# Kernel tuning notes

Measured on AMD Instinct MI355X. Metric: run time of the kernel, lower is better.

Reference implementation:

```python
import jax, jax.numpy as jnp
import numpy as np

B, C, H, W = 8, 64, 64, 64
CQ = C // 2

def setup_inputs() -> dict:
    key = jax.random.key(0)
    ks = jax.random.split(key, 10)
    s = 0.05
    return {
        "x": jax.random.normal(ks[0], (B, C, H, W), jnp.float32),
        "wq": jax.random.normal(ks[1], (CQ, C), jnp.float32) * s,
        "bq": jax.random.normal(ks[2], (CQ,), jnp.float32) * s,
        "wk": jax.random.normal(ks[3], (CQ, C), jnp.float32) * s,
        "bk": jax.random.normal(ks[4], (CQ,), jnp.float32) * s,
        "wv": jax.random.normal(ks[5], (C, C), jnp.float32) * s,
        "bv": jax.random.normal(ks[6], (C,), jnp.float32) * s,
        "wf": jax.random.normal(ks[7], (C, C), jnp.float32) * s,
        "bf": jax.random.normal(ks[8], (C,), jnp.float32) * s,
        "gamma": jnp.ones((1,), jnp.float32),
    }

def _conv1x1(w, b, x):
    # 1x1 conv == channel matmul: [O,C] x [B,C,H,W] -> [B,O,H,W]
    return jnp.einsum('oc,bchw->bohw', w, x) + b[None, :, None, None]

def reference(x, wq, bq, wk, bk, wv, bv, wf, bf, gamma):
    b, c, h, w = x.shape
    n = h * w
    q = _conv1x1(wq, bq, x).reshape(b, -1, n)   # [B, C/2, N]
    k = _conv1x1(wk, bk, x).reshape(b, -1, n)   # [B, C/2, N]
    v = _conv1x1(wv, bv, x).reshape(b, c, n)    # [B, C,   N]
    scale = 1.0 / jnp.sqrt(jnp.float32(n))
    energy = jnp.einsum('bcn,bcm->bnm', q, k) * scale  # [B, N, N]
    attn = jax.nn.softmax(energy, axis=-1)
    out = jnp.einsum('bcm,bnm->bcn', v, attn)          # V @ attn^T
    out = out.reshape(b, c, h, w)
    out = _conv1x1(wf, bf, out)
    return gamma[0] * out + x
```

## Files before the change

### kernel.cpp

```cpp
#include <hip/hip_runtime.h>

typedef unsigned short u16;
typedef unsigned int   u32;
typedef __bf16  bf16x8 __attribute__((ext_vector_type(8)));
typedef float   f32x16 __attribute__((ext_vector_type(16)));
typedef u32     u32x4  __attribute__((ext_vector_type(4)));

#define NN  4096
#define CCH 64
#define CQ  32
#define K1S 0.0225421092623961f

__device__ __forceinline__ u16 bfc(float a) { return __builtin_bit_cast(u16, (__bf16)a); }

__device__ __forceinline__ u32 e2pk_s(float a, float b, float& ps) {
  float ea, eb; u32 r;
  asm("v_exp_f32 %0, %1" : "=v"(ea) : "v"(a));
  asm("v_exp_f32 %0, %1" : "=v"(eb) : "v"(b));
  ps += ea + eb;
  asm("v_cvt_pk_bf16_f32 %0, %1, %2" : "=v"(r) : "v"(ea), "v"(eb));
  return r;
}

__device__ __forceinline__ void gload16(const void* g, void* l) {
  __builtin_amdgcn_global_load_lds((const __attribute__((address_space(1))) void*)g,
                                   (__attribute__((address_space(3))) void*)l, 16, 0, 0);
}


__global__ __launch_bounds__(512) void qkv_kernel(
    const float* __restrict__ x,
    const float* __restrict__ wq, const float* __restrict__ bq,
    const float* __restrict__ wk, const float* __restrict__ bk,
    const float* __restrict__ wv, const float* __restrict__ bv,
    u16* __restrict__ qT, char* __restrict__ kws, char* __restrict__ vws)
{
  __shared__ float xs[64][64];
  __shared__ u16 qls[64][34];
  __shared__ u16 kls[64][34];
  __shared__ u16 vls[64][66];
  const int bid = blockIdx.x;
  const int b = bid >> 6;
  const int chunk = bid & 63;
  const int nbase = chunk * 64;
  const int t = threadIdx.x, lane = t & 63, wid = t >> 6;

  {
    const float* xb = x + (size_t)b * CCH * NN + nbase;
    const int row = t >> 3, colq = (t & 7) * 2;
    float4 v0 = *(const float4*)(xb + (size_t)row * NN + colq * 4);
    float4 v1 = *(const float4*)(xb + (size_t)row * NN + colq * 4 + 4);
    float4* dst = (float4*)&xs[0][0];
    dst[row * 16 + colq]     = v0;
    dst[row * 16 + colq + 1] = v1;
  }
  __syncthreads();

  float xcol[64];
  #pragma unroll
  for (int c = 0; c < 64; ++c) xcol[c] = xs[c][lane];

  const float* w; const float* bias; float sc = 1.0f;
  const int sub = (wid & 1) * 16;
  if (wid < 2)      { w = wq + sub * 64; bias = bq + sub; sc = K1S; }
  else if (wid < 4) { w = wk + sub * 64; bias = bk + sub; }
  else              { w = wv + (wid - 4) * 16 * 64; bias = bv + (wid - 4) * 16; }

  #pragma unroll 2
  for (int i = 0; i < 16; ++i) {
    float a = bias[i];
    #pragma unroll
    for (int c = 0; c < 64; ++c) a = fmaf(w[i * 64 + c], xcol[c], a);
    a *= sc;
    u16 hv = bfc(a);
    if (wid < 2)      qls[lane][sub + i] = hv;
    else if (wid < 4) kls[lane][sub + i] = hv;
    else              vls[(wid - 4) * 16 + i][lane] = hv;
  }
  __syncthreads();

  u32* qdst = (u32*)(qT + ((size_t)b * NN + nbase) * CQ);
  #pragma unroll
  for (int jj = 0; jj < 2; ++jj) {
    int i = t + 512 * jj;
    int n = i >> 4, cp = i & 15;
    qdst[i] = *(const u32*)&qls[n][cp * 2];
  }
  u32* kimg = (u32*)(kws + ((size_t)b * 64 + chunk) * 4096);
  #pragma unroll
  for (int jj = 0; jj < 2; ++jj) {
    int i = t + 512 * jj;
    int reg = i >> 8, l = (i >> 2) & 63, j2 = i & 3;
    int s = reg >> 1, ks = reg & 1;
    int key = s * 32 + (l & 31);
    int ck  = ks * 16 + (l >> 5) * 8 + j2 * 2;
    kimg[i] = *(const u32*)&kls[key][ck];
  }
  u32* vimg = (u32*)(vws + ((size_t)b * 64 + chunk) * 8192);
  #pragma unroll
  for (int jj = 0; jj < 4; ++jj) {
    int i = t + 512 * jj;
    int reg = i >> 8, l = (i >> 2) & 63, j2 = i & 3;
    int s = reg >> 2, kb = (reg >> 1) & 1, ct = reg & 1;
    int c   = ct * 32 + (l & 31);
    int key = s * 32 + kb * 16 + (l >> 5) * 4 + (j2 >> 1) * 8 + (j2 & 1) * 2;
    vimg[i] = *(const u32*)&vls[c][key];
  }
}

template<int NSPLIT>
__global__ __launch_bounds__(256, 3) void attn_kernel(
    const u16* __restrict__ qT, const char* __restrict__ kws, const char* __restrict__ vws,
    u32* __restrict__ opart, float* __restrict__ lpart)
{
  constexpr int CH = 64 / NSPLIT;
  constexpr int MH = CH / 2;
  __shared__ __align__(16) char kbuf[2][8192];
  __shared__ __align__(16) char vbuf[2][16384];
  const int bid = blockIdx.x;
  const int b = bid & 7, qt = (bid >> 3) & 15, split = bid >> 7;
  const int t = threadIdx.x, lane = t & 63, wid = t >> 6;
  const int h = lane >> 5, c31 = lane & 31;

  const u16* qpA = qT + ((size_t)b * NN + qt * 256 + wid * 64 + c31) * CQ + h * 8;
  const bf16x8 qfA0 = *(const bf16x8*)(qpA);
  const bf16x8 qfA1 = *(const bf16x8*)(qpA + 16);
  const bf16x8 qfB0 = *(const bf16x8*)(qpA + 32 * CQ);
  const bf16x8 qfB1 = *(const bf16x8*)(qpA + 32 * CQ + 16);

  const char* ksrc = kws + ((size_t)b * 64 + split * CH) * 4096 + t * 16;
  const char* vsrc = vws + ((size_t)b * 64 + split * CH) * 8192 + t * 16;

  auto stage = [&](int buf, int m) {
    const char* kc = ksrc + (size_t)m * 8192;
    const char* vc = vsrc + (size_t)m * 16384;
    gload16(kc,         &kbuf[buf][wid * 1024]);
    gload16(kc + 4096,  &kbuf[buf][4096 + wid * 1024]);
    gload16(vc,         &vbuf[buf][wid * 1024]);
    gload16(vc + 4096,  &vbuf[buf][4096 + wid * 1024]);
    gload16(vc + 8192,  &vbuf[buf][8192 + wid * 1024]);
    gload16(vc + 12288, &vbuf[buf][12288 + wid * 1024]);
  };

  f32x16 accA0 = {}, accA1 = {}, accB0 = {}, accB1 = {};
  float lsumA = 0.f, lsumB = 0.f;
  const int lofs = lane * 16;

  stage(0, 0);

  #pragma unroll
  for (int m = 0; m < MH; ++m) {
    asm volatile("s_waitcnt vmcnt(0)" ::: "memory");
    __builtin_amdgcn_s_barrier();
    __builtin_amdgcn_sched_barrier(0);
    if (m + 1 < MH) stage((m + 1) & 1, m + 1);
    const int cur = m & 1;

    #pragma unroll
    for (int sub = 0; sub < 2; ++sub) {
      const char* kb = &kbuf[cur][sub * 4096];
      const char* vb = &vbuf[cur][sub * 8192];

      const bf16x8 kf0 = *(const bf16x8*)&kb[lofs];
      const bf16x8 kf1 = *(const bf16x8*)&kb[1024 + lofs];
      const bf16x8 kf2 = *(const bf16x8*)&kb[2048 + lofs];
      const bf16x8 kf3 = *(const bf16x8*)&kb[3072 + lofs];

      {
        f32x16 sA0, sA1;
        __builtin_amdgcn_s_setprio(1);
        sA0 = __builtin_amdgcn_mfma_f32_32x32x16_bf16(kf0, qfA0, (f32x16){}, 0, 0, 0);
        sA0 = __builtin_amdgcn_mfma_f32_32x32x16_bf16(kf1, qfA1, sA0, 0, 0, 0);
        sA1 = __builtin_amdgcn_mfma_f32_32x32x16_bf16(kf2, qfA0, (f32x16){}, 0, 0, 0);
        sA1 = __builtin_amdgcn_mfma_f32_32x32x16_bf16(kf3, qfA1, sA1, 0, 0, 0);
        __builtin_amdgcn_s_setprio(0);
        u32 pw[16] __attribute__((aligned(16)));
        #pragma unroll
        for (int r = 0; r < 16; r += 2) {
          pw[r >> 1]       = e2pk_s(sA0[r], sA0[r + 1], lsumA);
          pw[8 + (r >> 1)] = e2pk_s(sA1[r], sA1[r + 1], lsumA);
        }
        __builtin_amdgcn_s_setprio(1);
        #pragma unroll
        for (int s = 0; s < 2; ++s) {
          #pragma unroll
          for (int kb2 = 0; kb2 < 2; ++kb2) {
            const bf16x8 pf = __builtin_bit_cast(bf16x8, *(const u32x4*)&pw[s * 8 + kb2 * 4]);
            const bf16x8 vf0 = *(const bf16x8*)&vb[(s * 4 + kb2 * 2) * 1024 + lofs];
            const bf16x8 vf1 = *(const bf16x8*)&vb[(s * 4 + kb2 * 2 + 1) * 1024 + lofs];
            accA0 = __builtin_amdgcn_mfma_f32_32x32x16_bf16(vf0, pf, accA0, 0, 0, 0);
            accA1 = __builtin_amdgcn_mfma_f32_32x32x16_bf16(vf1, pf, accA1, 0, 0, 0);
          }
        }
        __builtin_amdgcn_s_setprio(0);
      }
      {
        f32x16 sB0, sB1;
        __builtin_amdgcn_s_setprio(1);
        sB0 = __builtin_amdgcn_mfma_f32_32x32x16_bf16(kf0, qfB0, (f32x16){}, 0, 0, 0);
        sB0 = __builtin_amdgcn_mfma_f32_32x32x16_bf16(kf1, qfB1, sB0, 0, 0, 0);
        sB1 = __builtin_amdgcn_mfma_f32_32x32x16_bf16(kf2, qfB0, (f32x16){}, 0, 0, 0);
        sB1 = __builtin_amdgcn_mfma_f32_32x32x16_bf16(kf3, qfB1, sB1, 0, 0, 0);
        __builtin_amdgcn_s_setprio(0);
        u32 pw[16] __attribute__((aligned(16)));
        #pragma unroll
        for (int r = 0; r < 16; r += 2) {
          pw[r >> 1]       = e2pk_s(sB0[r], sB0[r + 1], lsumB);
          pw[8 + (r >> 1)] = e2pk_s(sB1[r], sB1[r + 1], lsumB);
        }
        __builtin_amdgcn_s_setprio(1);
        #pragma unroll
        for (int s = 0; s < 2; ++s) {
          #pragma unroll
          for (int kb2 = 0; kb2 < 2; ++kb2) {
            const bf16x8 pf = __builtin_bit_cast(bf16x8, *(const u32x4*)&pw[s * 8 + kb2 * 4]);
            const bf16x8 vf0 = *(const bf16x8*)&vb[(s * 4 + kb2 * 2) * 1024 + lofs];
            const bf16x8 vf1 = *(const bf16x8*)&vb[(s * 4 + kb2 * 2 + 1) * 1024 + lofs];
            accB0 = __builtin_amdgcn_mfma_f32_32x32x16_bf16(vf0, pf, accB0, 0, 0, 0);
            accB1 = __builtin_amdgcn_mfma_f32_32x32x16_bf16(vf1, pf, accB1, 0, 0, 0);
          }
        }
        __builtin_amdgcn_s_setprio(0);
      }
    }
  }

  lsumA += __shfl_xor(lsumA, 32, 64);
  lsumB += __shfl_xor(lsumB, 32, 64);

  const int qt128 = qt * 2 + (wid >> 1);
  const size_t obase = ((size_t)(b * 32 + qt128) * NSPLIT + split) * 4096;
  #pragma unroll
  for (int j = 0; j < 2; ++j) {
    const int col = (wid & 1) * 64 + j * 32 + c31;
    #pragma unroll
    for (int ct = 0; ct < 2; ++ct) {
      const f32x16& a = j ? (ct ? accB1 : accB0) : (ct ? accA1 : accA0);
      #pragma unroll
      for (int g2 = 0; g2 < 4; ++g2) {
        #pragma unroll
        for (int b2 = 0; b2 < 2; ++b2) {
          int cp = ct * 16 + g2 * 4 + h * 2 + b2;
          float lo = a[g2 * 4 + b2 * 2], hi = a[g2 * 4 + b2 * 2 + 1];
          u32 pr; asm("v_cvt_pk_bf16_f32 %0, %1, %2" : "=v"(pr) : "v"(lo), "v"(hi));
          opart[obase + cp * 128 + col] = pr;
        }
      }
    }
    if (h == 0)
      lpart[((size_t)(b * 32 + qt128) * NSPLIT + split) * 128 + col] = j ? lsumB : lsumA;
  }
}

template<int NSPLIT>
__global__ __launch_bounds__(512) void combine_kernel(
    const u32* __restrict__ opart, const float* __restrict__ lpart,
    const float* __restrict__ x, const float* __restrict__ wf, const float* __restrict__ bfb,
    const float* __restrict__ gamma, float* __restrict__ out)
{
  __shared__ float ols[64][65];
  __shared__ float linv[64];
  const int bid = blockIdx.x;
  const int b = bid & 7, qt64 = bid >> 3;
  const int qt128 = qt64 >> 1, qh = qt64 & 1;
  const int t = threadIdx.x, lane = t & 63, wid = t >> 6;

  const u32* ob = opart + (size_t)(b * 32 + qt128) * NSPLIT * 4096 + qh * 64;
  #pragma unroll
  for (int jj = 0; jj < 4; ++jj) {
    int i = t + 512 * jj;
    int cp = i >> 6, q = i & 63;
    float lo = 0.f, hi = 0.f;
    #pragma unroll
    for (int s = 0; s < NSPLIT; ++s) {
      u32 a = ob[s * 4096 + cp * 128 + q];
      lo += __builtin_bit_cast(float, (a << 16));
      hi += __builtin_bit_cast(float, (a & 0xffff0000u));
    }
    ols[cp * 2][q]     = lo;
    ols[cp * 2 + 1][q] = hi;
  }
  if (t < 64) {
    const float* lp = lpart + (size_t)(b * 32 + qt128) * NSPLIT * 128 + qh * 64;
    float l = 0.f;
    #pragma unroll
    for (int s = 0; s < NSPLIT; ++s) l += lp[s * 128 + t];
    linv[t] = 1.f / l;
  }
  __syncthreads();

  const float oinv = linv[lane];
  float oc[64];
  #pragma unroll
  for (int c = 0; c < 64; ++c) oc[c] = ols[c][lane] * oinv;
  const float gm = gamma[0];
  const size_t nidx = (size_t)qt64 * 64 + lane;
  #pragma unroll
  for (int i = 0; i < 8; ++i) {
    const int o = wid * 8 + i;
    float a = bfb[o];
    #pragma unroll
    for (int c = 0; c < 64; ++c) a = fmaf(wf[o * 64 + c], oc[c], a);
    const size_t idx = ((size_t)b * CCH + o) * NN + nidx;
    out[idx] = gm * a + x[idx];
  }
}

extern "C" void kernel_launch(void* const* d_in, const int* in_sizes, int n_in,
                              void* d_out, int out_size, void* d_ws, size_t ws_size,
                              hipStream_t stream) {
  const float* x     = (const float*)d_in[0];
  const float* wq    = (const float*)d_in[1];
  const float* bq    = (const float*)d_in[2];
  const float* wk    = (const float*)d_in[3];
  const float* bk    = (const float*)d_in[4];
  const float* wv    = (const float*)d_in[5];
  const float* bv    = (const float*)d_in[6];
  const float* wf    = (const float*)d_in[7];
  const float* bf_   = (const float*)d_in[8];
  const float* gamma = (const float*)d_in[9];
  float* out = (float*)d_out;

  u16* qT   = (u16*)d_ws;
  char* kws = (char*)(qT + (size_t)8 * NN * CQ);
  char* vws = kws + (size_t)8 * 64 * 4096;
  u32* opart = (u32*)(vws + (size_t)8 * 64 * 8192);
  const size_t base = 2097152ull + 2097152ull + 4194304ull;
  const size_t need8 = base + 8ull * (4194304ull + 131072ull);
  const size_t need4 = base + 4ull * (4194304ull + 131072ull);

  qkv_kernel<<<dim3(512), dim3(512), 0, stream>>>(x, wq, bq, wk, bk, wv, bv, qT, kws, vws);
  if (ws_size >= need8) {
    float* lpart = (float*)(opart + (size_t)8 * 32 * 8 * 4096);
    attn_kernel<8><<<dim3(1024), dim3(256), 0, stream>>>(qT, kws, vws, opart, lpart);
    combine_kernel<8><<<dim3(512), dim3(512), 0, stream>>>(opart, lpart, x, wf, bf_, gamma, out);
  } else if (ws_size >= need4) {
    float* lpart = (float*)(opart + (size_t)8 * 32 * 4 * 4096);
    attn_kernel<4><<<dim3(512), dim3(256), 0, stream>>>(qT, kws, vws, opart, lpart);
    combine_kernel<4><<<dim3(512), dim3(512), 0, stream>>>(opart, lpart, x, wf, bf_, gamma, out);
  } else {
    float* lpart = (float*)(opart + (size_t)8 * 32 * 2 * 4096);
    attn_kernel<2><<<dim3(256), dim3(256), 0, stream>>>(qT, kws, vws, opart, lpart);
    combine_kernel<2><<<dim3(512), dim3(512), 0, stream>>>(opart, lpart, x, wf, bf_, gamma, out);
  }
}
```

Baseline: 94.41 us.

## Load K/V fragments directly to registers with double-buffered prefetch, drop LDS staging

Result: slower. 218.0 us (+130.9%).

```diff
diff --git a/kernel.cpp b/kernel.cpp
--- a/kernel.cpp
+++ b/kernel.cpp
@@ -20,11 +20,6 @@
   ps += ea + eb;
   asm("v_cvt_pk_bf16_f32 %0, %1, %2" : "=v"(r) : "v"(ea), "v"(eb));
   return r;
-}
-
-__device__ __forceinline__ void gload16(const void* g, void* l) {
-  __builtin_amdgcn_global_load_lds((const __attribute__((address_space(1))) void*)g,
-                                   (__attribute__((address_space(3))) void*)l, 16, 0, 0);
 }
 
 
@@ -109,14 +104,11 @@
 }
 
 template<int NSPLIT>
-__global__ __launch_bounds__(256, 3) void attn_kernel(
+__global__ __launch_bounds__(256, 2) void attn_kernel(
     const u16* __restrict__ qT, const char* __restrict__ kws, const char* __restrict__ vws,
     u32* __restrict__ opart, float* __restrict__ lpart)
 {
   constexpr int CH = 64 / NSPLIT;
-  constexpr int MH = CH / 2;
-  __shared__ __align__(16) char kbuf[2][8192];
-  __shared__ __align__(16) char vbuf[2][16384];
   const int bid = blockIdx.x;
   const int b = bid & 7, qt = (bid >> 3) & 15, split = bid >> 7;
   const int t = threadIdx.x, lane = t & 63, wid = t >> 6;
@@ -128,101 +120,88 @@
   const bf16x8 qfB0 = *(const bf16x8*)(qpA + 32 * CQ);
   const bf16x8 qfB1 = *(const bf16x8*)(qpA + 32 * CQ + 16);
 
-  const char* ksrc = kws + ((size_t)b * 64 + split * CH) * 4096 + t * 16;
-  const char* vsrc = vws + ((size_t)b * 64 + split * CH) * 8192 + t * 16;
-
-  auto stage = [&](int buf, int m) {
-    const char* kc = ksrc + (size_t)m * 8192;
-    const char* vc = vsrc + (size_t)m * 16384;
-    gload16(kc,         &kbuf[buf][wid * 1024]);
-    gload16(kc + 4096,  &kbuf[buf][4096 + wid * 1024]);
-    gload16(vc,         &vbuf[buf][wid * 1024]);
-    gload16(vc + 4096,  &vbuf[buf][4096 + wid * 1024]);
-    gload16(vc + 8192,  &vbuf[buf][8192 + wid * 1024]);
-    gload16(vc + 12288, &vbuf[buf][12288 + wid * 1024]);
-  };
+  const char* kcb = kws + ((size_t)b * 64 + split * CH) * 4096 + lane * 16;
+  const char* vcb = vws + ((size_t)b * 64 + split * CH) * 8192 + lane * 16;
 
   f32x16 accA0 = {}, accA1 = {}, accB0 = {}, accB1 = {};
   float lsumA = 0.f, lsumB = 0.f;
-  const int lofs = lane * 16;
-
-  stage(0, 0);
-
-  #pragma unroll
-  for (int m = 0; m < MH; ++m) {
-    asm volatile("s_waitcnt vmcnt(0)" ::: "memory");
-    __builtin_amdgcn_s_barrier();
-    __builtin_amdgcn_sched_barrier(0);
-    if (m + 1 < MH) stage((m + 1) & 1, m + 1);
-    const int cur = m & 1;
-
-    #pragma unroll
-    for (int sub = 0; sub < 2; ++sub) {
-      const char* kb = &kbuf[cur][sub * 4096];
-      const char* vb = &vbuf[cur][sub * 8192];
-
-      const bf16x8 kf0 = *(const bf16x8*)&kb[lofs];
-      const bf16x8 kf1 = *(const bf16x8*)&kb[1024 + lofs];
-      const bf16x8 kf2 = *(const bf16x8*)&kb[2048 + lofs];
-      const bf16x8 kf3 = *(const bf16x8*)&kb[3072 + lofs];
-
-      {
-        f32x16 sA0, sA1;
-        __builtin_amdgcn_s_setprio(1);
-        sA0 = __builtin_amdgcn_mfma_f32_32x32x16_bf16(kf0, qfA0, (f32x16){}, 0, 0, 0);
-        sA0 = __builtin_amdgcn_mfma_f32_32x32x16_bf16(kf1, qfA1, sA0, 0, 0, 0);
-        sA1 = __builtin_amdgcn_mfma_f32_32x32x16_bf16(kf2, qfA0, (f32x16){}, 0, 0, 0);
-        sA1 = __builtin_amdgcn_mfma_f32_32x32x16_bf16(kf3, qfA1, sA1, 0, 0, 0);
-        __builtin_amdgcn_s_setprio(0);
-        u32 pw[16] __attribute__((aligned(16)));
+
+  bf16x8 Ka[4], Va[8], Kb[4], Vb[8];
+
+  auto ldK = [&](int c, bf16x8 (&K)[4]) {
+    const char* p = kcb + (size_t)c * 4096;
+    #pragma unroll
+    for (int f = 0; f < 4; ++f) K[f] = *(const bf16x8*)(p + f * 1024);
+  };
+  auto ldV = [&](int c, bf16x8 (&V)[8]) {
+    const char* p = vcb + (size_t)c * 8192;
+    #pragma unroll
+    for (int f = 0; f < 8; ++f) V[f] = *(const bf16x8*)(p + f * 1024);
+  };
+
+  auto body = [&](const bf16x8 (&K)[4], const bf16x8 (&V)[8]) {
+    {
+      f32x16 s0, s1;
+      __builtin_amdgcn_s_setprio(1);
+      s0 = __builtin_amdgcn_mfma_f32_32x32x16_bf16(K[0], qfA0, (f32x16){}, 0, 0, 0);
+      s0 = __builtin_amdgcn_mfma_f32_32x32x16_bf16(K[1], qfA1, s0, 0, 0, 0);
+      s1 = __builtin_amdgcn_mfma_f32_32x32x16_bf16(K[2], qfA0, (f32x16){}, 0, 0, 0);
+      s1 = __builtin_amdgcn_mfma_f32_32x32x16_bf16(K[3], qfA1, s1, 0, 0, 0);
+      __builtin_amdgcn_s_setprio(0);
+      u32 pw[16] __attribute__((aligned(16)));
+      #pragma unroll
+      for (int r = 0; r < 16; r += 2) {
+        pw[r >> 1]       = e2pk_s(s0[r], s0[r + 1], lsumA);
+        pw[8 + (r >> 1)] = e2pk_s(s1[r], s1[r + 1], lsumA);
+      }
+      __builtin_amdgcn_s_setprio(1);
+      #pragma unroll
+      for (int s2 = 0; s2 < 2; ++s2) {
         #pragma unroll
-        for (int r = 0; r < 16; r += 2) {
-          pw[r >> 1]       = e2pk_s(sA0[r], sA0[r + 1], lsumA);
-          pw[8 + (r >> 1)] = e2pk_s(sA1[r], sA1[r + 1], lsumA);
+        for (int kb2 = 0; kb2 < 2; ++kb2) {
+          const bf16x8 pf = __builtin_bit_cast(bf16x8, *(const u32x4*)&pw[s2 * 8 + kb2 * 4]);
+          accA0 = __builtin_amdgcn_mfma_f32_32x32x16_bf16(V[s2 * 4 + kb2 * 2],     pf, accA0, 0, 0, 0);
+          accA1 = __builtin_amdgcn_mfma_f32_32x32x16_bf16(V[s2 * 4 + kb2 * 2 + 1], pf, accA1, 0, 0, 0);
         }
-        __builtin_amdgcn_s_setprio(1);
+      }
+      __builtin_amdgcn_s_setprio(0);
+    }
+    {
+      f32x16 s0, s1;
+      __builtin_amdgcn_s_setprio(1);
+      s0 = __builtin_amdgcn_mfma_f32_32x32x16_bf16(K[0], qfB0, (f32x16){}, 0, 0, 0);
+      s0 = __builtin_amdgcn_mfma_f32_32x32x16_bf16(K[1], qfB1, s0, 0, 0, 0);
+      s1 = __builtin_amdgcn_mfma_f32_32x32x16_bf16(K[2], qfB0, (f32x16){}, 0, 0, 0);
+      s1 = __builtin_amdgcn_mfma_f32_32x32x16_bf16(K[3], qfB1, s1, 0, 0, 0);
+      __builtin_amdgcn_s_setprio(0);
+      u32 pw[16] __attribute__((aligned(16)));
+      #pragma unroll
+      for (int r = 0; r < 16; r += 2) {
+        pw[r >> 1]       = e2pk_s(s0[r], s0[r + 1], lsumB);
+        pw[8 + (r >> 1)] = e2pk_s(s1[r], s1[r + 1], lsumB);
+      }
+      __builtin_amdgcn_s_setprio(1);
+      #pragma unroll
+      for (int s2 = 0; s2 < 2; ++s2) {
         #pragma unroll
-        for (int s = 0; s < 2; ++s) {
-          #pragma unroll
-          for (int kb2 = 0; kb2 < 2; ++kb2) {
-            const bf16x8 pf = __builtin_bit_cast(bf16x8, *(const u32x4*)&pw[s * 8 + kb2 * 4]);
-            const bf16x8 vf0 = *(const bf16x8*)&vb[(s * 4 + kb2 * 2) * 1024 + lofs];
-            const bf16x8 vf1 = *(const bf16x8*)&vb[(s * 4 + kb2 * 2 + 1) * 1024 + lofs];
-            accA0 = __builtin_amdgcn_mfma_f32_32x32x16_bf16(vf0, pf, accA0, 0, 0, 0);
-            accA1 = __builtin_amdgcn_mfma_f32_32x32x16_bf16(vf1, pf, accA1, 0, 0, 0);
-          }
+        for (int kb2 = 0; kb2 < 2; ++kb2) {
+          const bf16x8 pf = __builtin_bit_cast(bf16x8, *(const u32x4*)&pw[s2 * 8 + kb2 * 4]);
+          accB0 = __builtin_amdgcn_mfma_f32_32x32x16_bf16(V[s2 * 4 + kb2 * 2],     pf, accB0, 0, 0, 0);
+          accB1 = __builtin_amdgcn_mfma_f32_32x32x16_bf16(V[s2 * 4 + kb2 * 2 + 1], pf, accB1, 0, 0, 0);
         }
-        __builtin_amdgcn_s_setprio(0);
-      }
-      {
-        f32x16 sB0, sB1;
-        __builtin_amdgcn_s_setprio(1);
-        sB0 = __builtin_amdgcn_mfma_f32_32x32x16_bf16(kf0, qfB0, (f32x16){}, 0, 0, 0);
-        sB0 = __builtin_amdgcn_mfma_f32_32x32x16_bf16(kf1, qfB1, sB0, 0, 0, 0);
-        sB1 = __builtin_amdgcn_mfma_f32_32x32x16_bf16(kf2, qfB0, (f32x16){}, 0, 0, 0);
-        sB1 = __builtin_amdgcn_mfma_f32_32x32x16_bf16(kf3, qfB1, sB1, 0, 0, 0);
-        __builtin_amdgcn_s_setprio(0);
-        u32 pw[16] __attribute__((aligned(16)));
-        #pragma unroll
-        for (int r = 0; r < 16; r += 2) {
-          pw[r >> 1]       = e2pk_s(sB0[r], sB0[r + 1], lsumB);
-          pw[8 + (r >> 1)] = e2pk_s(sB1[r], sB1[r + 1], lsumB);
-        }
-        __builtin_amdgcn_s_setprio(1);
-        #pragma unroll
-        for (int s = 0; s < 2; ++s) {
-          #pragma unroll
-          for (int kb2 = 0; kb2 < 2; ++kb2) {
-            const bf16x8 pf = __builtin_bit_cast(bf16x8, *(const u32x4*)&pw[s * 8 + kb2 * 4]);
-            const bf16x8 vf0 = *(const bf16x8*)&vb[(s * 4 + kb2 * 2) * 1024 + lofs];
-            const bf16x8 vf1 = *(const bf16x8*)&vb[(s * 4 + kb2 * 2 + 1) * 1024 + lofs];
-            accB0 = __builtin_amdgcn_mfma_f32_32x32x16_bf16(vf0, pf, accB0, 0, 0, 0);
-            accB1 = __builtin_amdgcn_mfma_f32_32x32x16_bf16(vf1, pf, accB1, 0, 0, 0);
-          }
-        }
-        __builtin_amdgcn_s_setprio(0);
-      }
+      }
+      __builtin_amdgcn_s_setprio(0);
     }
+  };
+
+  ldK(0, Ka); ldV(0, Va);
+  ldK(1, Kb); ldV(1, Vb);
+
+  for (int it = 0; it < CH; it += 2) {
+    body(Ka, Va);
+    if (it + 2 < CH) { ldK(it + 2, Ka); ldV(it + 2, Va); }
+    body(Kb, Vb);
+    if (it + 3 < CH) { ldK(it + 3, Kb); ldV(it + 3, Vb); }
   }
 
   lsumA += __shfl_xor(lsumA, 32, 64);
@@ -326,15 +305,10 @@
   char* vws = kws + (size_t)8 * 64 * 4096;
   u32* opart = (u32*)(vws + (size_t)8 * 64 * 8192);
   const size_t base = 2097152ull + 2097152ull + 4194304ull;
-  const size_t need8 = base + 8ull * (4194304ull + 131072ull);
   const size_t need4 = base + 4ull * (4194304ull + 131072ull);
 
   qkv_kernel<<<dim3(512), dim3(512), 0, stream>>>(x, wq, bq, wk, bk, wv, bv, qT, kws, vws);
-  if (ws_size >= need8) {
-    float* lpart = (float*)(opart + (size_t)8 * 32 * 8 * 4096);
-    attn_kernel<8><<<dim3(1024), dim3(256), 0, stream>>>(qT, kws, vws, opart, lpart);
-    combine_kernel<8><<<dim3(512), dim3(512), 0, stream>>>(opart, lpart, x, wf, bf_, gamma, out);
-  } else if (ws_size >= need4) {
+  if (ws_size >= need4) {
     float* lpart = (float*)(opart + (size_t)8 * 32 * 4 * 4096);
     attn_kernel<4><<<dim3(512), dim3(256), 0, stream>>>(qT, kws, vws, opart, lpart);
     combine_kernel<4><<<dim3(512), dim3(512), 0, stream>>>(opart, lpart, x, wf, bf_, gamma, out);
```
